# Kernel tuning notes

Measured on AMD Instinct MI355X. Metric: run time of the kernel, lower is better.

Reference implementation:

```python
import jax, jax.numpy as jnp
import numpy as np

D_EMB = 768
N_HEADS = 12
D_K = D_EMB // N_HEADS


def setup_inputs() -> dict:
    key = jax.random.key(0)
    k0, k1, k2, k3, k4 = jax.random.split(key, 5)
    B, S = 2, 4096
    scale = 1.0 / np.sqrt(D_EMB)
    return {
        "inputs": jax.random.normal(k0, (B, S, D_EMB), dtype=jnp.float32),
        "Wq": jax.random.normal(k1, (D_EMB, D_EMB), dtype=jnp.float32) * scale,
        "Wk": jax.random.normal(k2, (D_EMB, D_EMB), dtype=jnp.float32) * scale,
        "Wv": jax.random.normal(k3, (D_EMB, D_EMB), dtype=jnp.float32) * scale,
        "Wo": jax.random.normal(k4, (D_EMB, D_EMB), dtype=jnp.float32) * scale,
    }


def reference(inputs, Wq, Wk, Wv, Wo):
    B, S, _ = inputs.shape
    def split_heads(x):  # [B,S,E] -> [B,H,S,dk]
        return x.reshape(B, S, N_HEADS, D_K).transpose(0, 2, 1, 3)
    q = split_heads(inputs @ Wq)
    k = split_heads(inputs @ Wk)
    v = split_heads(inputs @ Wv)
    scores = jnp.einsum("bhqd,bhkd->bhqk", q, k) / jnp.sqrt(
        jnp.asarray(D_K, dtype=inputs.dtype)
    )
    attn = jax.nn.softmax(scores, axis=-1)
    out = jnp.einsum("bhqk,bhkd->bhqd", attn, v)
    out = out.transpose(0, 2, 1, 3).reshape(B, S, D_EMB)
    return out @ Wo
```

## Files before the change

kernel.cpp:

```cpp
#include <hip/hip_runtime.h>

#define D_EMB 768
#define NH 12
#define DK 64
#define NB 2
#define SS 4096
#define E3 (3*D_EMB)
#define MM (NB*SS)

typedef unsigned short u16;
typedef __attribute__((ext_vector_type(8))) __bf16 bf16x8;
typedef __attribute__((ext_vector_type(4))) float f32x4;
typedef __attribute__((ext_vector_type(4))) unsigned int u32x4;

static __device__ __forceinline__ u16 f2bf(float f) {
  unsigned u = __builtin_bit_cast(unsigned, f);
  u += 0x7fffu + ((u >> 16) & 1u);
  return (u16)(u >> 16);
}
static __device__ __forceinline__ f32x4 mfma16(bf16x8 a, bf16x8 b, f32x4 c) {
  return __builtin_amdgcn_mfma_f32_16x16x32_bf16(a, b, c, 0, 0, 0);
}
static __device__ __forceinline__ float exp2_fast(float x) {
#if __has_builtin(__builtin_amdgcn_exp2f)
  return __builtin_amdgcn_exp2f(x);
#else
  return __builtin_exp2f(x);
#endif
}
static __device__ __forceinline__ float rcp_fast(float x) {
#if __has_builtin(__builtin_amdgcn_rcpf)
  return __builtin_amdgcn_rcpf(x);
#else
  return 1.f / x;
#endif
}
static __device__ __forceinline__ void gload_lds16(const u16* g, u16* l) {
  __builtin_amdgcn_global_load_lds((const __attribute__((address_space(1))) void*)g,
                                   (__attribute__((address_space(3))) void*)l, 16, 0, 0);
}

__global__ __launch_bounds__(256) void cast_kernel(const float* __restrict__ in,
                                                   u16* __restrict__ out, int n) {
  int i = (blockIdx.x * 256 + threadIdx.x) * 4;
  if (i + 3 < n) {
    float4 v = *(const float4*)(in + i);
    out[i + 0] = f2bf(v.x);
    out[i + 1] = f2bf(v.y);
    out[i + 2] = f2bf(v.z);
    out[i + 3] = f2bf(v.w);
  }
}

__global__ __launch_bounds__(256) void transpose_cast_w(const float* __restrict__ W,
                                                        u16* __restrict__ WT, float scale) {
  __shared__ float tile[32][33];
  int kb = blockIdx.y * 32, nb = blockIdx.x * 32;
  int tx = threadIdx.x, ty = threadIdx.y;
#pragma unroll
  for (int i = 0; i < 4; i++)
    tile[ty + i * 8][tx] = W[(size_t)(kb + ty + i * 8) * D_EMB + nb + tx];
  __syncthreads();
#pragma unroll
  for (int i = 0; i < 4; i++)
    WT[(size_t)(nb + ty + i * 8) * D_EMB + kb + tx] = f2bf(tile[tx][ty + i * 8] * scale);
}

__global__ __launch_bounds__(256) void transpose_v(const u16* __restrict__ QKV,
                                                   u16* __restrict__ VT) {
  __shared__ u16 tile[32][33];
  int bh = blockIdx.z;
  int b = bh / NH, h = bh % NH;
  int sb = blockIdx.x * 32, db = blockIdx.y * 32;
  int tx = threadIdx.x, ty = threadIdx.y;
  const u16* src = QKV + (size_t)(b * SS) * E3 + 2 * D_EMB + h * DK;
  u16* dst = VT + (size_t)bh * DK * SS;
#pragma unroll
  for (int i = 0; i < 4; i++)
    tile[ty + i * 8][tx] = src[(size_t)(sb + ty + i * 8) * E3 + db + tx];
  __syncthreads();
  int s = sb + tx;
  int k6 = s & 63;
  int p = (s & ~63) | (k6 & 0x23) | ((k6 & 0x0C) << 1) | ((k6 & 0x10) >> 2);
#pragma unroll
  for (int i = 0; i < 4; i++)
    dst[(size_t)(db + ty + i * 8) * SS + p] = tile[tx][ty + i * 8];
}

template <int OUTF32>
__global__ __launch_bounds__(256) void gemm_bt(const u16* __restrict__ A,
                                               const u16* __restrict__ Bt,
                                               void* __restrict__ Cout,
                                               int M, int N, int K, float scale) {
  __shared__ __align__(16) u16 As[128 * 32];
  __shared__ __align__(16) u16 Bs[128 * 32];
  int tid = threadIdx.x;
  int wave = tid >> 6, lane = tid & 63;
  int g = lane >> 4, nIdx = lane & 15;
  int m0 = blockIdx.y * 128, n0 = blockIdx.x * 128;
  int wm = (wave >> 1) * 64, wn = (wave & 1) * 64;

  f32x4 acc[4][4] = {};

  int row = tid >> 2, co = (tid & 3) * 8;
  int row2 = row + 64;

  for (int k0 = 0; k0 < K; k0 += 32) {
    __syncthreads();
    gload_lds16(A  + (size_t)(m0 + row)  * K + k0 + co, As + row  * 32 + co);
    gload_lds16(Bt + (size_t)(n0 + row)  * K + k0 + co, Bs + row  * 32 + co);
    gload_lds16(A  + (size_t)(m0 + row2) * K + k0 + co, As + row2 * 32 + co);
    gload_lds16(Bt + (size_t)(n0 + row2) * K + k0 + co, Bs + row2 * 32 + co);
    __syncthreads();

    bf16x8 af[4], bfr[4];
#pragma unroll
    for (int i = 0; i < 4; i++)
      af[i] = *(const bf16x8*)(As + (wm + i * 16 + nIdx) * 32 + g * 8);
#pragma unroll
    for (int j = 0; j < 4; j++)
      bfr[j] = *(const bf16x8*)(Bs + (wn + j * 16 + nIdx) * 32 + g * 8);
#pragma unroll
    for (int i = 0; i < 4; i++)
#pragma unroll
      for (int j = 0; j < 4; j++)
        acc[i][j] = mfma16(af[i], bfr[j], acc[i][j]);
  }

#pragma unroll
  for (int i = 0; i < 4; i++)
#pragma unroll
    for (int j = 0; j < 4; j++)
#pragma unroll
      for (int r = 0; r < 4; r++) {
        int rr = m0 + wm + i * 16 + g * 4 + r;
        int cc = n0 + wn + j * 16 + nIdx;
        float v = acc[i][j][r] * scale;
        if (OUTF32)
          ((float*)Cout)[(size_t)rr * N + cc] = v;
        else
          ((u16*)Cout)[(size_t)rr * N + cc] = f2bf(v);
      }
}

__global__ __launch_bounds__(256, 3) void flash(const u16* __restrict__ QKV,
                                                const u16* __restrict__ VT,
                                                u16* __restrict__ O) {
  __shared__ __align__(16) u16 Ks[64 * 72];
  __shared__ __align__(16) u16 Vs[64 * 72];

  int b = blockIdx.z, h = blockIdx.y;
  int q0 = blockIdx.x * 128;
  int tid = threadIdx.x, w = tid >> 6, l = tid & 63;
  int g = l >> 4, n = l & 15;

  const u16* Qbase = QKV + (size_t)(b * SS + q0 + w * 32) * E3 + h * DK;
  const u16* Kbase = QKV + (size_t)(b * SS) * E3 + D_EMB + h * DK;
  const u16* VTb = VT + (size_t)(b * NH + h) * DK * SS;

  bf16x8 qf[2][2];
#pragma unroll
  for (int qg = 0; qg < 2; qg++)
#pragma unroll
    for (int hf = 0; hf < 2; hf++)
      qf[qg][hf] = *(const bf16x8*)(Qbase + (size_t)(qg * 16 + n) * E3 + hf * 32 + g * 8);

  f32x4 o_acc[2][4] = {};
  f32x4 l_acc[2] = {};
  u32x4 onev = {0x3F803F80u, 0x3F803F80u, 0x3F803F80u, 0x3F803F80u};
  bf16x8 aone = __builtin_bit_cast(bf16x8, onev);

  int sr = tid >> 3, sc = (tid & 7) * 8;
  const u16* Kg  = Kbase + (size_t)sr * E3 + sc;
  const u16* Kg2 = Kbase + (size_t)(sr + 32) * E3 + sc;
  const u16* Vg  = VTb + (size_t)sr * SS + sc;
  const u16* Vg2 = VTb + (size_t)(sr + 32) * SS + sc;
  u16* KsW  = Ks + sr * 72 + sc;
  u16* KsW2 = KsW + 32 * 72;
  u16* VsW  = Vs + sr * 72 + sc;
  u16* VsW2 = VsW + 32 * 72;

  uint4 ka = *(const uint4*)Kg;
  uint4 kb = *(const uint4*)Kg2;
  uint4 va = *(const uint4*)Vg;
  uint4 vb = *(const uint4*)Vg2;

  for (int kt = 0; kt < SS / 64; kt++) {
    __syncthreads();
    *(uint4*)KsW  = ka;
    *(uint4*)KsW2 = kb;
    *(uint4*)VsW  = va;
    *(uint4*)VsW2 = vb;
    __syncthreads();

    if (kt < SS / 64 - 1) {
      size_t ko = (size_t)(kt + 1) * 64 * E3;
      int vo = (kt + 1) * 64;
      ka = *(const uint4*)(Kg + ko);
      kb = *(const uint4*)(Kg2 + ko);
      va = *(const uint4*)(Vg + vo);
      vb = *(const uint4*)(Vg2 + vo);
    }

    f32x4 C[2][4];
#pragma unroll
    for (int j = 0; j < 4; j++) {
      bf16x8 kf0 = *(const bf16x8*)(Ks + (j * 16 + n) * 72 + g * 8);
      bf16x8 kf1 = *(const bf16x8*)(Ks + (j * 16 + n) * 72 + 32 + g * 8);
#pragma unroll
      for (int qg = 0; qg < 2; qg++) {
        f32x4 t = {};
        t = mfma16(kf0, qf[qg][0], t);
        t = mfma16(kf1, qf[qg][1], t);
        C[qg][j] = t;
      }
    }

    u32x4 Bw[2][2];
#pragma unroll
    for (int qg = 0; qg < 2; qg++) {
#pragma unroll
      for (int j = 0; j < 4; j++) {
        float p0 = exp2_fast(C[qg][j][0]);
        float p1 = exp2_fast(C[qg][j][1]);
        float p2 = exp2_fast(C[qg][j][2]);
        float p3 = exp2_fast(C[qg][j][3]);
        unsigned lo = __builtin_amdgcn_perm(__builtin_bit_cast(unsigned, p1),
                                            __builtin_bit_cast(unsigned, p0), 0x07060302u);
        unsigned hi = __builtin_amdgcn_perm(__builtin_bit_cast(unsigned, p3),
                                            __builtin_bit_cast(unsigned, p2), 0x07060302u);
        Bw[qg][j >> 1][(j & 1) * 2]     = lo;
        Bw[qg][j >> 1][(j & 1) * 2 + 1] = hi;
      }
      bf16x8 B0 = __builtin_bit_cast(bf16x8, Bw[qg][0]);
      bf16x8 B1 = __builtin_bit_cast(bf16x8, Bw[qg][1]);
      l_acc[qg] = mfma16(aone, B0, l_acc[qg]);
      l_acc[qg] = mfma16(aone, B1, l_acc[qg]);
    }

#pragma unroll
    for (int dt = 0; dt < 4; dt++) {
      bf16x8 vf0 = *(const bf16x8*)(Vs + (dt * 16 + n) * 72 + g * 8);
      bf16x8 vf1 = *(const bf16x8*)(Vs + (dt * 16 + n) * 72 + 32 + g * 8);
#pragma unroll
      for (int qg = 0; qg < 2; qg++) {
        o_acc[qg][dt] = mfma16(vf0, __builtin_bit_cast(bf16x8, Bw[qg][0]), o_acc[qg][dt]);
        o_acc[qg][dt] = mfma16(vf1, __builtin_bit_cast(bf16x8, Bw[qg][1]), o_acc[qg][dt]);
      }
    }
  }

#pragma unroll
  for (int qg = 0; qg < 2; qg++) {
    float rl = rcp_fast(l_acc[qg][0]);
    u16* Ob = O + (size_t)(b * SS + q0 + w * 32 + qg * 16 + n) * D_EMB + h * DK;
#pragma unroll
    for (int dt = 0; dt < 4; dt++) {
      unsigned w0 = (unsigned)f2bf(o_acc[qg][dt][0] * rl) |
                    ((unsigned)f2bf(o_acc[qg][dt][1] * rl) << 16);
      unsigned w1 = (unsigned)f2bf(o_acc[qg][dt][2] * rl) |
                    ((unsigned)f2bf(o_acc[qg][dt][3] * rl) << 16);
      *(unsigned*)(Ob + dt * 16 + g * 4) = w0;
      *(unsigned*)(Ob + dt * 16 + g * 4 + 2) = w1;
    }
  }
}

extern "C" void kernel_launch(void* const* d_in, const int* in_sizes, int n_in,
                              void* d_out, int out_size, void* d_ws, size_t ws_size,
                              hipStream_t stream) {
  const float* X  = (const float*)d_in[0];
  const float* Wq = (const float*)d_in[1];
  const float* Wk = (const float*)d_in[2];
  const float* Wv = (const float*)d_in[3];
  const float* Wo = (const float*)d_in[4];
  float* out = (float*)d_out;

  u16* Xb    = (u16*)d_ws;
  u16* WTqkv = Xb + (size_t)MM * D_EMB;
  u16* WoT   = WTqkv + (size_t)E3 * D_EMB;
  u16* QKV   = WoT + (size_t)D_EMB * D_EMB;
  u16* VT    = QKV + (size_t)MM * E3;
  u16* Ob    = VT + (size_t)NB * NH * DK * SS;

  dim3 tb(32, 8);
  cast_kernel<<<(MM * D_EMB) / 1024, 256, 0, stream>>>(X, Xb, MM * D_EMB);
  transpose_cast_w<<<dim3(24, 24), tb, 0, stream>>>(Wq, WTqkv, 0.125f * 1.4426950408889634f);
  transpose_cast_w<<<dim3(24, 24), tb, 0, stream>>>(Wk, WTqkv + (size_t)D_EMB * D_EMB, 1.0f);
  transpose_cast_w<<<dim3(24, 24), tb, 0, stream>>>(Wv, WTqkv + (size_t)2 * D_EMB * D_EMB, 1.0f);
  transpose_cast_w<<<dim3(24, 24), tb, 0, stream>>>(Wo, WoT, 1.0f);

  gemm_bt<0><<<dim3(E3 / 128, MM / 128), 256, 0, stream>>>(Xb, WTqkv, (void*)QKV,
                                                           MM, E3, D_EMB, 1.0f);
  transpose_v<<<dim3(SS / 32, 2, NB * NH), tb, 0, stream>>>(QKV, VT);
  flash<<<dim3(SS / 128, NH, NB), 256, 0, stream>>>(QKV, VT, Ob);
  gemm_bt<1><<<dim3(D_EMB / 128, MM / 128), 256, 0, stream>>>(Ob, WoT, (void*)out,
                                                              MM, D_EMB, D_EMB, 1.0f);
}
```

Baseline: 284.4 us.

## Split flash KV range across wave pairs with 64-row Q tiles and merge

The flash kernel now gives each wave 64 query rows instead of 32. The two wave pairs each process half of the key sequence in separate LDS buffers, and at the end the partial output accumulators and row sums are merged through shared memory. Each loaded K/V fragment now feeds more MFMAs and each pair loads only half the keys, at the cost of more registers, a larger LDS footprint that may lower occupancy, and a final reduction step. Separately, the four weight transpose-cast launches are merged into one launch.

```diff
diff --git a/kernel.cpp b/kernel.cpp
--- a/kernel.cpp
+++ b/kernel.cpp
@@ -52,9 +52,17 @@
   }
 }
 
-__global__ __launch_bounds__(256) void transpose_cast_w(const float* __restrict__ W,
-                                                        u16* __restrict__ WT, float scale) {
+__global__ __launch_bounds__(256) void transpose_cast_all(const float* __restrict__ Wq,
+                                                          const float* __restrict__ Wk,
+                                                          const float* __restrict__ Wv,
+                                                          const float* __restrict__ Wo,
+                                                          u16* __restrict__ WTqkv,
+                                                          u16* __restrict__ WoT, float qscale) {
   __shared__ float tile[32][33];
+  int z = blockIdx.z;
+  const float* W = (z == 0) ? Wq : (z == 1) ? Wk : (z == 2) ? Wv : Wo;
+  u16* WT = (z < 3) ? WTqkv + (size_t)z * D_EMB * D_EMB : WoT;
+  float scale = (z == 0) ? qscale : 1.0f;
   int kb = blockIdx.y * 32, nb = blockIdx.x * 32;
   int tx = threadIdx.x, ty = threadIdx.y;
 #pragma unroll
@@ -146,122 +154,156 @@
 __global__ __launch_bounds__(256, 3) void flash(const u16* __restrict__ QKV,
                                                 const u16* __restrict__ VT,
                                                 u16* __restrict__ O) {
-  __shared__ __align__(16) u16 Ks[64 * 72];
-  __shared__ __align__(16) u16 Vs[64 * 72];
+  __shared__ __align__(16) u16 smem[18432];
 
   int b = blockIdx.z, h = blockIdx.y;
   int q0 = blockIdx.x * 128;
   int tid = threadIdx.x, w = tid >> 6, l = tid & 63;
   int g = l >> 4, n = l & 15;
-
-  const u16* Qbase = QKV + (size_t)(b * SS + q0 + w * 32) * E3 + h * DK;
-  const u16* Kbase = QKV + (size_t)(b * SS) * E3 + D_EMB + h * DK;
+  int qh = w & 1, st = w >> 1;
+
   const u16* VTb = VT + (size_t)(b * NH + h) * DK * SS;
-
-  bf16x8 qf[2][2];
-#pragma unroll
-  for (int qg = 0; qg < 2; qg++)
+  u16* pKs = smem + st * 9216;
+  u16* pVs = pKs + 4608;
+
+  const u16* Qbase = QKV + (size_t)(b * SS + q0 + qh * 64) * E3 + h * DK;
+  bf16x8 qf[4][2];
+#pragma unroll
+  for (int qg = 0; qg < 4; qg++)
 #pragma unroll
     for (int hf = 0; hf < 2; hf++)
       qf[qg][hf] = *(const bf16x8*)(Qbase + (size_t)(qg * 16 + n) * E3 + hf * 32 + g * 8);
 
-  f32x4 o_acc[2][4] = {};
-  f32x4 l_acc[2] = {};
+  f32x4 o_acc[4][4] = {};
+  float lsum[4] = {0.f, 0.f, 0.f, 0.f};
   u32x4 onev = {0x3F803F80u, 0x3F803F80u, 0x3F803F80u, 0x3F803F80u};
   bf16x8 aone = __builtin_bit_cast(bf16x8, onev);
 
-  int sr = tid >> 3, sc = (tid & 7) * 8;
-  const u16* Kg  = Kbase + (size_t)sr * E3 + sc;
-  const u16* Kg2 = Kbase + (size_t)(sr + 32) * E3 + sc;
-  const u16* Vg  = VTb + (size_t)sr * SS + sc;
-  const u16* Vg2 = VTb + (size_t)(sr + 32) * SS + sc;
-  u16* KsW  = Ks + sr * 72 + sc;
-  u16* KsW2 = KsW + 32 * 72;
-  u16* VsW  = Vs + sr * 72 + sc;
-  u16* VsW2 = VsW + 32 * 72;
-
-  uint4 ka = *(const uint4*)Kg;
-  uint4 kb = *(const uint4*)Kg2;
-  uint4 va = *(const uint4*)Vg;
-  uint4 vb = *(const uint4*)Vg2;
-
-  for (int kt = 0; kt < SS / 64; kt++) {
+  int rL = l >> 3, cL = l & 7;
+  const u16* g0;
+  size_t rstep, tstep;
+  u16* sW;
+  if ((w & 1) == 0) {
+    g0 = QKV + ((size_t)(b * SS) + st * 2048 + rL) * E3 + D_EMB + h * DK + cL * 8;
+    rstep = (size_t)8 * E3;
+    tstep = (size_t)64 * E3;
+    sW = pKs + rL * 72 + cL * 8;
+  } else {
+    g0 = VTb + (size_t)rL * SS + st * 2048 + cL * 8;
+    rstep = (size_t)8 * SS;
+    tstep = 64;
+    sW = pVs + rL * 72 + cL * 8;
+  }
+
+  uint4 pf[8];
+#pragma unroll
+  for (int i = 0; i < 8; i++)
+    pf[i] = *(const uint4*)(g0 + i * rstep);
+
+  for (int kt = 0; kt < 32; kt++) {
     __syncthreads();
-    *(uint4*)KsW  = ka;
-    *(uint4*)KsW2 = kb;
-    *(uint4*)VsW  = va;
-    *(uint4*)VsW2 = vb;
+#pragma unroll
+    for (int i = 0; i < 8; i++)
+      *(uint4*)(sW + i * 576) = pf[i];
     __syncthreads();
 
-    if (kt < SS / 64 - 1) {
-      size_t ko = (size_t)(kt + 1) * 64 * E3;
-      int vo = (kt + 1) * 64;
-      ka = *(const uint4*)(Kg + ko);
-      kb = *(const uint4*)(Kg2 + ko);
-      va = *(const uint4*)(Vg + vo);
-      vb = *(const uint4*)(Vg2 + vo);
+    if (kt < 31) {
+      const u16* gn = g0 + (size_t)(kt + 1) * tstep;
+#pragma unroll
+      for (int i = 0; i < 8; i++)
+        pf[i] = *(const uint4*)(gn + i * rstep);
     }
 
-    f32x4 C[2][4];
-#pragma unroll
-    for (int j = 0; j < 4; j++) {
-      bf16x8 kf0 = *(const bf16x8*)(Ks + (j * 16 + n) * 72 + g * 8);
-      bf16x8 kf1 = *(const bf16x8*)(Ks + (j * 16 + n) * 72 + 32 + g * 8);
-#pragma unroll
-      for (int qg = 0; qg < 2; qg++) {
-        f32x4 t = {};
-        t = mfma16(kf0, qf[qg][0], t);
-        t = mfma16(kf1, qf[qg][1], t);
-        C[qg][j] = t;
+#pragma unroll
+    for (int s = 0; s < 2; s++) {
+      bf16x8 kf[2][2];
+#pragma unroll
+      for (int jj = 0; jj < 2; jj++)
+#pragma unroll
+        for (int hf = 0; hf < 2; hf++)
+          kf[jj][hf] = *(const bf16x8*)(pKs + ((2 * s + jj) * 16 + n) * 72 + hf * 32 + g * 8);
+
+#pragma unroll
+      for (int p = 0; p < 2; p++) {
+        f32x4 C[2][2];
+#pragma unroll
+        for (int q2 = 0; q2 < 2; q2++) {
+          int qg = 2 * p + q2;
+#pragma unroll
+          for (int jj = 0; jj < 2; jj++) {
+            f32x4 t = {};
+            t = mfma16(kf[jj][0], qf[qg][0], t);
+            t = mfma16(kf[jj][1], qf[qg][1], t);
+            C[q2][jj] = t;
+          }
+        }
+        u32x4 Bw[2];
+#pragma unroll
+        for (int q2 = 0; q2 < 2; q2++)
+#pragma unroll
+          for (int jj = 0; jj < 2; jj++) {
+            float p0 = exp2_fast(C[q2][jj][0]);
+            float p1 = exp2_fast(C[q2][jj][1]);
+            float p2 = exp2_fast(C[q2][jj][2]);
+            float p3 = exp2_fast(C[q2][jj][3]);
+            Bw[q2][jj * 2] = __builtin_amdgcn_perm(__builtin_bit_cast(unsigned, p1),
+                                                   __builtin_bit_cast(unsigned, p0), 0x07060302u);
+            Bw[q2][jj * 2 + 1] = __builtin_amdgcn_perm(__builtin_bit_cast(unsigned, p3),
+                                                       __builtin_bit_cast(unsigned, p2), 0x07060302u);
+          }
+#pragma unroll
+        for (int q2 = 0; q2 < 2; q2++) {
+          f32x4 z = {};
+          z = mfma16(aone, __builtin_bit_cast(bf16x8, Bw[q2]), z);
+          lsum[2 * p + q2] += z[0];
+        }
+#pragma unroll
+        for (int dt = 0; dt < 4; dt++) {
+          bf16x8 vf = *(const bf16x8*)(pVs + (dt * 16 + n) * 72 + s * 32 + g * 8);
+#pragma unroll
+          for (int q2 = 0; q2 < 2; q2++)
+            o_acc[2 * p + q2][dt] = mfma16(vf, __builtin_bit_cast(bf16x8, Bw[q2]),
+                                           o_acc[2 * p + q2][dt]);
+        }
       }
     }
-
-    u32x4 Bw[2][2];
-#pragma unroll
-    for (int qg = 0; qg < 2; qg++) {
-#pragma unroll
-      for (int j = 0; j < 4; j++) {
-        float p0 = exp2_fast(C[qg][j][0]);
-        float p1 = exp2_fast(C[qg][j][1]);
-        float p2 = exp2_fast(C[qg][j][2]);
-        float p3 = exp2_fast(C[qg][j][3]);
-        unsigned lo = __builtin_amdgcn_perm(__builtin_bit_cast(unsigned, p1),
-                                            __builtin_bit_cast(unsigned, p0), 0x07060302u);
-        unsigned hi = __builtin_amdgcn_perm(__builtin_bit_cast(unsigned, p3),
-                                            __builtin_bit_cast(unsigned, p2), 0x07060302u);
-        Bw[qg][j >> 1][(j & 1) * 2]     = lo;
-        Bw[qg][j >> 1][(j & 1) * 2 + 1] = hi;
+  }
+
+  __syncthreads();
+
+  float* dumpF = (float*)smem;
+  if (w >= 2) {
+    float* dst = dumpF + ((size_t)((w - 2) * 64 + l)) * 68;
+#pragma unroll
+    for (int qg = 0; qg < 4; qg++)
+#pragma unroll
+      for (int dt = 0; dt < 4; dt++)
+        *(f32x4*)(dst + (qg * 4 + dt) * 4) = o_acc[qg][dt];
+    f32x4 lv = {lsum[0], lsum[1], lsum[2], lsum[3]};
+    *(f32x4*)(dst + 64) = lv;
+  }
+  __syncthreads();
+  if (w < 2) {
+    float* src = dumpF + ((size_t)(w * 64 + l)) * 68;
+#pragma unroll
+    for (int qg = 0; qg < 4; qg++)
+#pragma unroll
+      for (int dt = 0; dt < 4; dt++)
+        o_acc[qg][dt] += *(f32x4*)(src + (qg * 4 + dt) * 4);
+    f32x4 lv = *(f32x4*)(src + 64);
+#pragma unroll
+    for (int qg = 0; qg < 4; qg++) {
+      float rl = rcp_fast(lsum[qg] + lv[qg]);
+      u16* Obp = O + (size_t)(b * SS + q0 + w * 64 + qg * 16 + n) * D_EMB + h * DK;
+#pragma unroll
+      for (int dt = 0; dt < 4; dt++) {
+        uint2 pk;
+        pk.x = (unsigned)f2bf(o_acc[qg][dt][0] * rl) |
+               ((unsigned)f2bf(o_acc[qg][dt][1] * rl) << 16);
+        pk.y = (unsigned)f2bf(o_acc[qg][dt][2] * rl) |
+               ((unsigned)f2bf(o_acc[qg][dt][3] * rl) << 16);
+        *(uint2*)(Obp + dt * 16 + g * 4) = pk;
       }
-      bf16x8 B0 = __builtin_bit_cast(bf16x8, Bw[qg][0]);
-      bf16x8 B1 = __builtin_bit_cast(bf16x8, Bw[qg][1]);
-      l_acc[qg] = mfma16(aone, B0, l_acc[qg]);
-      l_acc[qg] = mfma16(aone, B1, l_acc[qg]);
-    }
-
-#pragma unroll
-    for (int dt = 0; dt < 4; dt++) {
-      bf16x8 vf0 = *(const bf16x8*)(Vs + (dt * 16 + n) * 72 + g * 8);
-      bf16x8 vf1 = *(const bf16x8*)(Vs + (dt * 16 + n) * 72 + 32 + g * 8);
-#pragma unroll
-      for (int qg = 0; qg < 2; qg++) {
-        o_acc[qg][dt] = mfma16(vf0, __builtin_bit_cast(bf16x8, Bw[qg][0]), o_acc[qg][dt]);
-        o_acc[qg][dt] = mfma16(vf1, __builtin_bit_cast(bf16x8, Bw[qg][1]), o_acc[qg][dt]);
-      }
-    }
-  }
-
-#pragma unroll
-  for (int qg = 0; qg < 2; qg++) {
-    float rl = rcp_fast(l_acc[qg][0]);
-    u16* Ob = O + (size_t)(b * SS + q0 + w * 32 + qg * 16 + n) * D_EMB + h * DK;
-#pragma unroll
-    for (int dt = 0; dt < 4; dt++) {
-      unsigned w0 = (unsigned)f2bf(o_acc[qg][dt][0] * rl) |
-                    ((unsigned)f2bf(o_acc[qg][dt][1] * rl) << 16);
-      unsigned w1 = (unsigned)f2bf(o_acc[qg][dt][2] * rl) |
-                    ((unsigned)f2bf(o_acc[qg][dt][3] * rl) << 16);
-      *(unsigned*)(Ob + dt * 16 + g * 4) = w0;
-      *(unsigned*)(Ob + dt * 16 + g * 4 + 2) = w1;
     }
   }
 }
@@ -285,11 +327,8 @@
 
   dim3 tb(32, 8);
   cast_kernel<<<(MM * D_EMB) / 1024, 256, 0, stream>>>(X, Xb, MM * D_EMB);
-  transpose_cast_w<<<dim3(24, 24), tb, 0, stream>>>(Wq, WTqkv, 0.125f * 1.4426950408889634f);
-  transpose_cast_w<<<dim3(24, 24), tb, 0, stream>>>(Wk, WTqkv + (size_t)D_EMB * D_EMB, 1.0f);
-  transpose_cast_w<<<dim3(24, 24), tb, 0, stream>>>(Wv, WTqkv + (size_t)2 * D_EMB * D_EMB, 1.0f);
-  transpose_cast_w<<<dim3(24, 24), tb, 0, stream>>>(Wo, WoT, 1.0f);
-
+  transpose_cast_all<<<dim3(24, 24, 4), tb, 0, stream>>>(Wq, Wk, Wv, Wo, WTqkv, WoT,
+                                                         0.125f * 1.4426950408889634f);
   gemm_bt<0><<<dim3(E3 / 128, MM / 128), 256, 0, stream>>>(Xb, WTqkv, (void*)QKV,
                                                            MM, E3, D_EMB, 1.0f);
   transpose_v<<<dim3(SS / 32, 2, NB * NH), tb, 0, stream>>>(QKV, VT);
```

After: 410.1 us. +44.2%, slower.
